# Kernel optimization log

Hardware: AMD Instinct MI355X
Metric: run time of the kernel (lower is better)

The kernel has to match this reference:

```python
import jax, jax.numpy as jnp
import numpy as np

B, T, I, H = 64, 2048, 256, 256

def setup_inputs() -> dict:
    key = jax.random.key(0)
    k1, k2, k3, k4, k5 = jax.random.split(key, 5)
    s = 1.0 / np.sqrt(H)
    return {
        "x": jax.random.normal(k1, (B, T, I), dtype=jnp.float32),
        "weight_ih": jax.random.normal(k2, (3 * H, I), dtype=jnp.float32) * s,
        "weight_hh": jax.random.normal(k3, (3 * H, H), dtype=jnp.float32) * s,
        "bias_ih": jax.random.normal(k4, (3 * H,), dtype=jnp.float32) * s,
        "bias_hh": jax.random.normal(k5, (3 * H,), dtype=jnp.float32) * s,
    }

def reference(x, weight_ih, weight_hh, bias_ih, bias_hh):
    # x: [B, T, I] (batch_first). Permute to time-major, scan GRU cell.
    xt = jnp.swapaxes(x, 0, 1)  # [T, B, I]
    # Precompute input-side gate projections for all timesteps: [T, B, 3H]
    gi_all = jnp.einsum('tbi,gi->tbg', xt, weight_ih) + bias_ih
    h0 = jnp.zeros((x.shape[0], H), dtype=x.dtype)

    def step(h, gi):
        gh = h @ weight_hh.T + bias_hh  # [B, 3H]
        i_r, i_z, i_n = jnp.split(gi, 3, axis=-1)
        h_r, h_z, h_n = jnp.split(gh, 3, axis=-1)
        r = jax.nn.sigmoid(i_r + h_r)
        z = jax.nn.sigmoid(i_z + h_z)
        n = jnp.tanh(i_n + r * h_n)
        h_new = (1.0 - z) * n + z * h
        return h_new, None

    h_final, _ = jax.lax.scan(step, h0, gi_all)
    return h_final  # return_sequences=False, return_state=False -> last hidden [B, H]
```

## Files before the change

### kernel.cpp

```cpp
#include <hip/hip_runtime.h>
#include <hip/hip_fp16.h>

typedef _Float16 h2 __attribute__((ext_vector_type(2)));
typedef _Float16 h8 __attribute__((ext_vector_type(8)));
typedef float f4 __attribute__((ext_vector_type(4)));
typedef unsigned int uv16 __attribute__((ext_vector_type(16)));

static constexpr int TT = 2048;
static constexpr int BB = 64;
static constexpr int II = 256;
static constexpr int HH = 256;
static constexpr int G3 = 768;

static __device__ __forceinline__ unsigned int pk2(float a, float b) {
    return __builtin_bit_cast(unsigned int, __builtin_amdgcn_cvt_pkrtz(a, b));
}
static __device__ __forceinline__ float fdot2u(unsigned int w, unsigned int h, float acc) {
    return __builtin_amdgcn_fdot2(__builtin_bit_cast(h2, w), __builtin_bit_cast(h2, h), acc, false);
}
template <int OFF>
static __device__ __forceinline__ float swz_add(float s) {
    int v = __builtin_amdgcn_ds_swizzle(__builtin_bit_cast(int, s), OFF);
    return s + __builtin_bit_cast(float, v);
}
static __device__ __forceinline__ float dot16(uv16 W, uint4 A, uint4 B, uint4 C, uint4 D, float s) {
    float a0 = 0.f, a1 = 0.f, a2 = 0.f, a3 = 0.f;
    a0 = fdot2u(W[0],  A.x, a0); a1 = fdot2u(W[1],  A.y, a1);
    a2 = fdot2u(W[2],  A.z, a2); a3 = fdot2u(W[3],  A.w, a3);
    a0 = fdot2u(W[4],  B.x, a0); a1 = fdot2u(W[5],  B.y, a1);
    a2 = fdot2u(W[6],  B.z, a2); a3 = fdot2u(W[7],  B.w, a3);
    a0 = fdot2u(W[8],  C.x, a0); a1 = fdot2u(W[9],  C.y, a1);
    a2 = fdot2u(W[10], C.z, a2); a3 = fdot2u(W[11], C.w, a3);
    a0 = fdot2u(W[12], D.x, a0); a1 = fdot2u(W[13], D.y, a1);
    a2 = fdot2u(W[14], D.z, a2); a3 = fdot2u(W[15], D.w, a3);
    return s + ((a0 + a1) + (a2 + a3));
}

__global__ void cast_wih(const float* __restrict__ w, _Float16* __restrict__ o, int n) {
    int i = blockIdx.x * blockDim.x + threadIdx.x;
    if (i < n) o[i] = (_Float16)w[i];
}

__global__ void gi_gemm(const float* __restrict__ x, const _Float16* __restrict__ wih,
                        const float* __restrict__ bih, _Float16* __restrict__ gi) {
    const int lane = threadIdx.x & 63;
    const int wid  = threadIdx.x >> 6;
    const int gt   = blockIdx.x * 4 + wid;
    const int nt   = gt % 12;
    const int mt   = gt / 12;
    const int m0   = mt * 64;
    const int n0   = nt * 64;
    const int lr   = lane & 15;
    const int kg   = (lane >> 4) * 8;

    f4 acc[4][4] = {};

    #pragma unroll
    for (int kk = 0; kk < 256; kk += 32) {
        h8 af[4];
        h8 bf[4];
        #pragma unroll
        for (int m = 0; m < 4; ++m) {
            const float* ap = x + (size_t)(m0 + m * 16 + lr) * 256 + kk + kg;
            f4 lo = *(const f4*)ap;
            f4 hi = *(const f4*)(ap + 4);
            uint4 uu;
            uu.x = pk2(lo.x, lo.y);
            uu.y = pk2(lo.z, lo.w);
            uu.z = pk2(hi.x, hi.y);
            uu.w = pk2(hi.z, hi.w);
            af[m] = __builtin_bit_cast(h8, uu);
        }
        #pragma unroll
        for (int n = 0; n < 4; ++n) {
            bf[n] = *(const h8*)(wih + (size_t)(n0 + n * 16 + lr) * 256 + kk + kg);
        }
        #pragma unroll
        for (int m = 0; m < 4; ++m) {
            #pragma unroll
            for (int n = 0; n < 4; ++n) {
                acc[m][n] = __builtin_amdgcn_mfma_f32_16x16x32_f16(af[m], bf[n], acc[m][n], 0, 0, 0);
            }
        }
    }

    const int rg = (lane >> 4) * 4;
    #pragma unroll
    for (int n = 0; n < 4; ++n) {
        const int col = n0 + n * 16 + lr;
        const float bv = bih[col];
        #pragma unroll
        for (int m = 0; m < 4; ++m) {
            #pragma unroll
            for (int r = 0; r < 4; ++r) {
                const int row = m0 + m * 16 + rg + r;
                gi[(size_t)row * G3 + col] = (_Float16)(acc[m][n][r] + bv);
            }
        }
    }
}

__global__ __launch_bounds__(512, 2)
void gru_scan(
        const _Float16* __restrict__ gi, const float* __restrict__ whh,
        const float* __restrict__ bhh, float* __restrict__ out) {
    __shared__ alignas(16) unsigned int hpk[128];
    __shared__ float ghl[768];

    const int b     = blockIdx.x;
    const int tid   = threadIdx.x;
    const int sub   = tid & 1;
    const int rbase = (tid >> 1) * 3;

    auto loadw = [&](int j, int q) -> uv16 {
        const f4* wp = (const f4*)(whh + (size_t)(rbase + j) * 256 + sub * 128 + q * 32);
        uv16 W;
        #pragma unroll
        for (int i = 0; i < 8; ++i) {
            f4 v = wp[i];
            W[2 * i]     = pk2(v.x, v.y);
            W[2 * i + 1] = pk2(v.z, v.w);
        }
        return W;
    };
    const uv16 w00 = loadw(0,0), w01 = loadw(0,1), w02 = loadw(0,2), w03 = loadw(0,3);
    const uv16 w10 = loadw(1,0), w11 = loadw(1,1), w12 = loadw(1,2), w13 = loadw(1,3);
    const uv16 w20 = loadw(2,0), w21 = loadw(2,1), w22 = loadw(2,2), w23 = loadw(2,3);

    if (tid < 128) hpk[tid] = 0u;

    const _Float16* gb = gi + (size_t)b * TT * G3;
    float b_r = 0.f, b_z = 0.f, b_n = 0.f;
    float c_r = 0.f, c_z = 0.f, c_n = 0.f;
    float n_r = 0.f, n_z = 0.f, n_n = 0.f;
    float hcur = 0.f;
    if (tid < 256) {
        b_r = bhh[tid];
        b_z = bhh[256 + tid];
        b_n = bhh[512 + tid];
        c_r = (float)gb[tid];
        c_z = (float)gb[256 + tid];
        c_n = (float)gb[512 + tid];
        n_r = (float)gb[G3 + tid];
        n_z = (float)gb[G3 + 256 + tid];
        n_n = (float)gb[G3 + 512 + tid];
    }
    __syncthreads();

    for (int t = 0; t < TT; ++t) {
        float p_r = 0.f, p_z = 0.f, p_n = 0.f;
        if (tid < 256 && t + 2 < TT) {
            const _Float16* g2 = gb + (size_t)(t + 2) * G3;
            p_r = (float)g2[tid];
            p_z = (float)g2[256 + tid];
            p_n = (float)g2[512 + tid];
        }

        float s0 = 0.f, s1 = 0.f, s2 = 0.f;
        #define QBLOCK(q, W0, W1, W2)                                         \
        {                                                                     \
            const uint4* hp = (const uint4*)&hpk[sub * 64 + (q) * 16];        \
            const uint4 A = hp[0], B = hp[1], C = hp[2], D = hp[3];           \
            s0 = dot16(W0, A, B, C, D, s0);                                   \
            s1 = dot16(W1, A, B, C, D, s1);                                   \
            s2 = dot16(W2, A, B, C, D, s2);                                   \
        }
        QBLOCK(0, w00, w10, w20)
        QBLOCK(1, w01, w11, w21)
        QBLOCK(2, w02, w12, w22)
        QBLOCK(3, w03, w13, w23)
        #undef QBLOCK

        s0 = swz_add<0x041F>(s0);
        s1 = swz_add<0x041F>(s1);
        s2 = swz_add<0x041F>(s2);
        if (sub == 0) {
            ghl[rbase + 0] = s0;
            ghl[rbase + 1] = s1;
            ghl[rbase + 2] = s2;
        }
        __syncthreads();

        if (tid < 256) {
            const float xr = c_r + b_r + ghl[tid];
            const float xz = c_z + b_z + ghl[256 + tid];
            const float r = __builtin_amdgcn_rcpf(1.f + __expf(-xr));
            const float z = __builtin_amdgcn_rcpf(1.f + __expf(-xz));
            const float xn = c_n + r * (ghl[512 + tid] + b_n);
            const float th = 1.f - 2.f * __builtin_amdgcn_rcpf(__expf(2.f * xn) + 1.f);
            hcur = (1.f - z) * th + z * hcur;
            ((_Float16*)hpk)[tid] = (_Float16)hcur;
            c_r = n_r; c_z = n_z; c_n = n_n;
            n_r = p_r; n_z = p_z; n_n = p_n;
        }
        __syncthreads();
    }

    if (tid < 256) out[(size_t)b * HH + tid] = hcur;
}

extern "C" void kernel_launch(void* const* d_in, const int* in_sizes, int n_in,
                              void* d_out, int out_size, void* d_ws, size_t ws_size,
                              hipStream_t stream) {
    const float* x   = (const float*)d_in[0];
    const float* wih = (const float*)d_in[1];
    const float* whh = (const float*)d_in[2];
    const float* bih = (const float*)d_in[3];
    const float* bhh = (const float*)d_in[4];
    float* out = (float*)d_out;

    _Float16* wih_h = (_Float16*)d_ws;
    _Float16* gi    = (_Float16*)((char*)d_ws + 512 * 1024);

    cast_wih<<<768, 256, 0, stream>>>(wih, wih_h, G3 * II);
    gi_gemm<<<6144, 256, 0, stream>>>(x, wih_h, bih, gi);
    gru_scan<<<BB, 512, 0, stream>>>(gi, whh, bhh, out);
}
```

Baseline: 3.235 ms.

## Assign one hidden unit per thread and double-buffer h to drop a barrier

The recurrent scan now uses 256 threads, each owning a full hidden unit and holding all three gate rows of W_hh in registers as packed fp16. This removes the split-K swizzle reduction, the LDS staging of gate sums and one of the two per-step barriers. The hidden state is double-buffered in shared memory so a single barrier per timestep suffices. The trade-off is twice the dot-product work per thread and heavy register pressure (384 weight registers), which may cause spills or low occupancy.

New measurement: 6.027 ms. 1.86x slower.

```diff
diff --git a/kernel.cpp b/kernel.cpp
--- a/kernel.cpp
+++ b/kernel.cpp
@@ -17,11 +17,6 @@
 }
 static __device__ __forceinline__ float fdot2u(unsigned int w, unsigned int h, float acc) {
     return __builtin_amdgcn_fdot2(__builtin_bit_cast(h2, w), __builtin_bit_cast(h2, h), acc, false);
-}
-template <int OFF>
-static __device__ __forceinline__ float swz_add(float s) {
-    int v = __builtin_amdgcn_ds_swizzle(__builtin_bit_cast(int, s), OFF);
-    return s + __builtin_bit_cast(float, v);
 }
 static __device__ __forceinline__ float dot16(uv16 W, uint4 A, uint4 B, uint4 C, uint4 D, float s) {
     float a0 = 0.f, a1 = 0.f, a2 = 0.f, a3 = 0.f;
@@ -100,103 +95,82 @@
     }
 }
 
-__global__ __launch_bounds__(512, 2)
+__global__ __launch_bounds__(256, 1)
 void gru_scan(
         const _Float16* __restrict__ gi, const float* __restrict__ whh,
         const float* __restrict__ bhh, float* __restrict__ out) {
-    __shared__ alignas(16) unsigned int hpk[128];
-    __shared__ float ghl[768];
+    __shared__ alignas(16) unsigned int hpk[2][128];
 
-    const int b     = blockIdx.x;
-    const int tid   = threadIdx.x;
-    const int sub   = tid & 1;
-    const int rbase = (tid >> 1) * 3;
+    const int b   = blockIdx.x;
+    const int tid = threadIdx.x;
 
-    auto loadw = [&](int j, int q) -> uv16 {
-        const f4* wp = (const f4*)(whh + (size_t)(rbase + j) * 256 + sub * 128 + q * 32);
-        uv16 W;
+    uv16 W0[8], W1[8], W2[8];
+    #pragma unroll
+    for (int i = 0; i < 8; ++i) {
+        const f4* p0 = (const f4*)(whh + (size_t)tid * 256 + i * 32);
+        const f4* p1 = (const f4*)(whh + (size_t)(256 + tid) * 256 + i * 32);
+        const f4* p2 = (const f4*)(whh + (size_t)(512 + tid) * 256 + i * 32);
+        uv16 a, c, d;
         #pragma unroll
-        for (int i = 0; i < 8; ++i) {
-            f4 v = wp[i];
-            W[2 * i]     = pk2(v.x, v.y);
-            W[2 * i + 1] = pk2(v.z, v.w);
+        for (int k = 0; k < 8; ++k) {
+            f4 v0 = p0[k], v1 = p1[k], v2 = p2[k];
+            a[2 * k] = pk2(v0.x, v0.y); a[2 * k + 1] = pk2(v0.z, v0.w);
+            c[2 * k] = pk2(v1.x, v1.y); c[2 * k + 1] = pk2(v1.z, v1.w);
+            d[2 * k] = pk2(v2.x, v2.y); d[2 * k + 1] = pk2(v2.z, v2.w);
         }
-        return W;
-    };
-    const uv16 w00 = loadw(0,0), w01 = loadw(0,1), w02 = loadw(0,2), w03 = loadw(0,3);
-    const uv16 w10 = loadw(1,0), w11 = loadw(1,1), w12 = loadw(1,2), w13 = loadw(1,3);
-    const uv16 w20 = loadw(2,0), w21 = loadw(2,1), w22 = loadw(2,2), w23 = loadw(2,3);
+        W0[i] = a; W1[i] = c; W2[i] = d;
+    }
 
-    if (tid < 128) hpk[tid] = 0u;
+    const float b_r = bhh[tid];
+    const float b_z = bhh[256 + tid];
+    const float b_n = bhh[512 + tid];
+
+    if (tid < 128) { hpk[0][tid] = 0u; hpk[1][tid] = 0u; }
 
     const _Float16* gb = gi + (size_t)b * TT * G3;
-    float b_r = 0.f, b_z = 0.f, b_n = 0.f;
-    float c_r = 0.f, c_z = 0.f, c_n = 0.f;
-    float n_r = 0.f, n_z = 0.f, n_n = 0.f;
+    float c_r = (float)gb[tid];
+    float c_z = (float)gb[256 + tid];
+    float c_n = (float)gb[512 + tid];
+    float n_r = (float)gb[G3 + tid];
+    float n_z = (float)gb[G3 + 256 + tid];
+    float n_n = (float)gb[G3 + 512 + tid];
     float hcur = 0.f;
-    if (tid < 256) {
-        b_r = bhh[tid];
-        b_z = bhh[256 + tid];
-        b_n = bhh[512 + tid];
-        c_r = (float)gb[tid];
-        c_z = (float)gb[256 + tid];
-        c_n = (float)gb[512 + tid];
-        n_r = (float)gb[G3 + tid];
-        n_z = (float)gb[G3 + 256 + tid];
-        n_n = (float)gb[G3 + 512 + tid];
-    }
     __syncthreads();
 
     for (int t = 0; t < TT; ++t) {
         float p_r = 0.f, p_z = 0.f, p_n = 0.f;
-        if (tid < 256 && t + 2 < TT) {
+        if (t + 2 < TT) {
             const _Float16* g2 = gb + (size_t)(t + 2) * G3;
             p_r = (float)g2[tid];
             p_z = (float)g2[256 + tid];
             p_n = (float)g2[512 + tid];
         }
 
+        const uint4* hb = (const uint4*)hpk[t & 1];
         float s0 = 0.f, s1 = 0.f, s2 = 0.f;
-        #define QBLOCK(q, W0, W1, W2)                                         \
-        {                                                                     \
-            const uint4* hp = (const uint4*)&hpk[sub * 64 + (q) * 16];        \
-            const uint4 A = hp[0], B = hp[1], C = hp[2], D = hp[3];           \
-            s0 = dot16(W0, A, B, C, D, s0);                                   \
-            s1 = dot16(W1, A, B, C, D, s1);                                   \
-            s2 = dot16(W2, A, B, C, D, s2);                                   \
+        #pragma unroll
+        for (int i = 0; i < 8; ++i) {
+            const uint4 A = hb[4 * i], B = hb[4 * i + 1], C = hb[4 * i + 2], D = hb[4 * i + 3];
+            s0 = dot16(W0[i], A, B, C, D, s0);
+            s1 = dot16(W1[i], A, B, C, D, s1);
+            s2 = dot16(W2[i], A, B, C, D, s2);
         }
-        QBLOCK(0, w00, w10, w20)
-        QBLOCK(1, w01, w11, w21)
-        QBLOCK(2, w02, w12, w22)
-        QBLOCK(3, w03, w13, w23)
-        #undef QBLOCK
 
-        s0 = swz_add<0x041F>(s0);
-        s1 = swz_add<0x041F>(s1);
-        s2 = swz_add<0x041F>(s2);
-        if (sub == 0) {
-            ghl[rbase + 0] = s0;
-            ghl[rbase + 1] = s1;
-            ghl[rbase + 2] = s2;
-        }
-        __syncthreads();
+        const float xr = c_r + b_r + s0;
+        const float xz = c_z + b_z + s1;
+        const float r = __builtin_amdgcn_rcpf(1.f + __expf(-xr));
+        const float z = __builtin_amdgcn_rcpf(1.f + __expf(-xz));
+        const float xn = c_n + r * (s2 + b_n);
+        const float th = 1.f - 2.f * __builtin_amdgcn_rcpf(__expf(2.f * xn) + 1.f);
+        hcur = (1.f - z) * th + z * hcur;
 
-        if (tid < 256) {
-            const float xr = c_r + b_r + ghl[tid];
-            const float xz = c_z + b_z + ghl[256 + tid];
-            const float r = __builtin_amdgcn_rcpf(1.f + __expf(-xr));
-            const float z = __builtin_amdgcn_rcpf(1.f + __expf(-xz));
-            const float xn = c_n + r * (ghl[512 + tid] + b_n);
-            const float th = 1.f - 2.f * __builtin_amdgcn_rcpf(__expf(2.f * xn) + 1.f);
-            hcur = (1.f - z) * th + z * hcur;
-            ((_Float16*)hpk)[tid] = (_Float16)hcur;
-            c_r = n_r; c_z = n_z; c_n = n_n;
-            n_r = p_r; n_z = p_z; n_n = p_n;
-        }
+        ((_Float16*)hpk[(t + 1) & 1])[tid] = (_Float16)hcur;
+        c_r = n_r; c_z = n_z; c_n = n_n;
+        n_r = p_r; n_z = p_z; n_n = p_n;
         __syncthreads();
     }
 
-    if (tid < 256) out[(size_t)b * HH + tid] = hcur;
+    out[(size_t)b * HH + tid] = hcur;
 }
 
 extern "C" void kernel_launch(void* const* d_in, const int* in_sizes, int n_in,
@@ -214,5 +188,5 @@
 
     cast_wih<<<768, 256, 0, stream>>>(wih, wih_h, G3 * II);
     gi_gemm<<<6144, 256, 0, stream>>>(x, wih_h, bih, gi);
-    gru_scan<<<BB, 512, 0, stream>>>(gi, whh, bhh, out);
+    gru_scan<<<BB, 256, 0, stream>>>(gi, whh, bhh, out);
 }
```
